# Performance work log

Hardware: AMD Instinct MI355X
Metric: run time of the kernel (lower is better)

Reference implementation:

```python
import jax, jax.numpy as jnp
import numpy as np

EPS_BN = 1e-5
EPS_LN = 1e-5
EPS_L2 = 1e-12


def adder2d(x, w, stride):
    """AdderNet pseudo-conv: out = -sum |x_patch - w| (negative L1 distance).
    x: (N, Cin, H, W); w: (Cout, Cin, kh, kw); no padding, no bias.
    Loops only over the small fixed kernel footprint (<=12 positions) to avoid
    materializing the full im2col L1 tensor at once.
    """
    N, Cin, H, W = x.shape
    Cout, _, kh, kw = w.shape
    sh, sw = stride
    Ho = (H - kh) // sh + 1
    Wo = (W - kw) // sw + 1
    out = jnp.zeros((N, Ho, Wo, Cout), dtype=x.dtype)
    for i in range(kh):
        for j in range(kw):
            # strided slice of the input for this kernel tap: (N, Cin, Ho, Wo)
            xs = x[:, :, i:i + sh * Ho:sh, j:j + sw * Wo:sw]
            xs = jnp.transpose(xs, (0, 2, 3, 1))          # (N, Ho, Wo, Cin)
            wt = w[:, :, i, j]                            # (Cout, Cin)
            # |x - w| summed over Cin -> (N, Ho, Wo, Cout)
            out = out - jnp.abs(xs[:, :, :, None, :] - wt[None, None, None, :, :]).sum(-1)
    return jnp.transpose(out, (0, 3, 1, 2))               # (N, Cout, Ho, Wo)


def bn_relu(x, gamma, beta):
    # training-mode BatchNorm2d (batch statistics, biased var) + ReLU
    mean = x.mean(axis=(0, 2, 3), keepdims=True)
    var = x.var(axis=(0, 2, 3), keepdims=True)
    y = (x - mean) * jax.lax.rsqrt(var + EPS_BN)
    y = y * gamma[None, :, None, None] + beta[None, :, None, None]
    return jax.nn.relu(y)


def setup_inputs() -> dict:
    key = jax.random.key(0)
    ks = jax.random.split(key, 8)
    N = 16
    x = jax.random.normal(ks[0], (N, 1, 196, 3), dtype=jnp.float32)
    w1 = jax.random.normal(ks[1], (128, 1, 6, 1), dtype=jnp.float32) * 0.1
    w2 = jax.random.normal(ks[2], (256, 128, 6, 1), dtype=jnp.float32) * 0.05
    w3 = jax.random.normal(ks[3], (384, 256, 6, 2), dtype=jnp.float32) * 0.05
    g1, b1 = jnp.ones((128,), jnp.float32), jnp.zeros((128,), jnp.float32)
    g2, b2 = jnp.ones((256,), jnp.float32), jnp.zeros((256,), jnp.float32)
    g3, b3 = jnp.ones((384,), jnp.float32), jnp.zeros((384,), jnp.float32)
    Wfc = jax.random.normal(ks[4], (6, 16128), dtype=jnp.float32) * (1.0 / np.sqrt(16128))
    bfc = jax.random.normal(ks[5], (6,), dtype=jnp.float32) * 0.01
    return {"x": x, "w1": w1, "g1": g1, "b1": b1, "w2": w2, "g2": g2, "b2": b2,
            "w3": w3, "g3": g3, "b3": b3, "Wfc": Wfc, "bfc": bfc}


def reference(x, w1, g1, b1, w2, g2, b2, w3, g3, b3, Wfc, bfc):
    h = bn_relu(adder2d(x, w1, (2, 1)), g1, b1)   # (N,128,96,3)
    h = bn_relu(adder2d(h, w2, (2, 1)), g2, b2)   # (N,256,46,3)
    h = bn_relu(adder2d(h, w3, (2, 1)), g3, b3)   # (N,384,21,2)
    h = h.reshape(h.shape[0], -1)                  # (N,16128)
    h = h @ Wfc.T + bfc                            # (N,6)
    # nn.LayerNorm(x.size()) normalizes over ALL dims (batch included), weight=1 bias=0
    mu = h.mean()
    var = h.var()
    h = (h - mu) * jax.lax.rsqrt(var + EPS_LN)
    # F.normalize: per-row L2 normalization
    norm = jnp.sqrt((h * h).sum(axis=1, keepdims=True))
    return h / jnp.maximum(norm, EPS_L2)
```

## Files before the change

kernel.cpp:

```cpp
#include <hip/hip_runtime.h>
#include <math.h>

#define DEVINL __device__ __forceinline__

DEVINL float absadd(float a, float b) {
  float t;
  asm("v_add_f32 %0, |%1|, |%2|" : "=v"(t) : "v"(a), "v"(b));
  return t;
}

template<int NWAVES>
DEVINL void block_reduce_2d(double& a, double& b) {
  #pragma unroll
  for (int off = 32; off > 0; off >>= 1) {
    a += __shfl_down(a, off, 64);
    b += __shfl_down(b, off, 64);
  }
  __shared__ double sa[NWAVES], sb[NWAVES];
  const int tid = threadIdx.x;
  const int wid = tid >> 6;
  if ((tid & 63) == 0) { sa[wid] = a; sb[wid] = b; }
  __syncthreads();
  if (tid == 0) {
    double ta = 0.0, tb = 0.0;
    #pragma unroll
    for (int w = 0; w < NWAVES; ++w) { ta += sa[w]; tb += sb[w]; }
    a = ta; b = tb;
  }
}

__global__ __launch_bounds__(256) void k_conv1(
    const float* __restrict__ x, const float* __restrict__ w1,
    const float* __restrict__ g1, const float* __restrict__ b1,
    float* __restrict__ h1) {
  __shared__ float xlds[9408];
  const int co = blockIdx.x;
  const int tid = threadIdx.x;
  {
    float4* xd = (float4*)xlds;
    const float4* xs = (const float4*)x;
    #pragma unroll
    for (int k = 0; k < 10; ++k) {
      const int f = tid + k * 256;
      if (f < 2352) xd[f] = xs[f];
    }
  }
  float wv[6];
  #pragma unroll
  for (int i = 0; i < 6; ++i) wv[i] = w1[co * 6 + i];
  __syncthreads();

  float vals[18];
  double s = 0.0, sq = 0.0;
  #pragma unroll
  for (int k = 0; k < 18; ++k) {
    const int p = tid + k * 256;
    const int n = p / 288;
    const int r = p - n * 288;
    const int ho = r / 3;
    const int wo = r - ho * 3;
    const float* xb = xlds + n * 588 + (2 * ho) * 3 + wo;
    float e0 = xb[0]  - wv[0];
    float e1 = xb[3]  - wv[1];
    float e2 = xb[6]  - wv[2];
    float e3 = xb[9]  - wv[3];
    float e4 = xb[12] - wv[4];
    float e5 = xb[15] - wv[5];
    const float t0 = absadd(e0, e1);
    const float t1 = absadd(e2, e3);
    const float t2 = absadd(e4, e5);
    const float v = -((t0 + t1) + t2);
    vals[k] = v;
    s += (double)v;
    sq += (double)v * (double)v;
  }
  block_reduce_2d<4>(s, sq);
  __shared__ float ssc, ssh;
  if (tid == 0) {
    const double mean = s * (1.0 / 4608.0);
    const double var  = sq * (1.0 / 4608.0) - mean * mean;
    const float rstd = (float)rsqrt(var + 1e-5);
    const float sc = g1[co] * rstd;
    ssc = sc;
    ssh = b1[co] - (float)mean * sc;
  }
  __syncthreads();
  const float sc = ssc, sh = ssh;
  #pragma unroll
  for (int k = 0; k < 18; ++k) {
    const int p = tid + k * 256;
    const int n = p / 288;
    const int r = p - n * 288;
    const int ho = r / 3;
    const int wo = r - ho * 3;
    h1[((n * 128 + co) * 96 + ho) * 3 + wo] = fmaxf(0.f, fmaf(vals[k], sc, sh));
  }
}

__global__ __launch_bounds__(192) void k_conv2p(
    const float* __restrict__ h1, const float* __restrict__ w2,
    float* __restrict__ part2) {
  __shared__ float wlds[512];
  __shared__ float4 xbuf[2][584];
  const int bx = blockIdx.x;
  const int kc = bx & 7;
  const int rbx = bx >> 3;
  const int cg = rbx & 63;
  const int nh = rbx >> 6;
  const int co0 = cg * 4, ci0 = kc * 16, n0 = nh * 8;
  const int tid = threadIdx.x;
  #pragma unroll
  for (int f = tid; f < 512; f += 192) {
    const int cil = f >> 5, rem = f & 31, c = rem >> 3, kk = rem & 7;
    wlds[f] = (kk < 6) ? w2[(co0 + c) * 768 + (ci0 + cil) * 6 + kk] : 0.f;
  }
  const bool active = tid < 184;
  const int n = tid / 23, hp = tid - n * 23;

  int s_lds[3], s_g[3];
  #pragma unroll
  for (int k = 0; k < 3; ++k) {
    const int f = tid + k * 192;
    const int nn = f / 72, j = f - nn * 72;
    s_lds[k] = nn * 73 + j;
    s_g[k]   = (n0 + nn) * 9216 + j;
  }
  const float4* h1v = (const float4*)h1;

  float acc[4][6];
  #pragma unroll
  for (int c = 0; c < 4; ++c)
    #pragma unroll
    for (int o = 0; o < 6; ++o) acc[c][o] = 0.f;

  float4 r[3];
  #pragma unroll
  for (int k = 0; k < 3; ++k) r[k] = h1v[s_g[k] + ci0 * 72];
  #pragma unroll
  for (int k = 0; k < 3; ++k) xbuf[0][s_lds[k]] = r[k];
  #pragma unroll
  for (int k = 0; k < 3; ++k) r[k] = h1v[s_g[k] + (ci0 + 1) * 72];
  __syncthreads();

  const float4* wl4 = (const float4*)wlds;
  #pragma unroll 1
  for (int ci = 0; ci < 16; ++ci) {
    const float4* cur = xbuf[ci & 1];
    if (ci + 1 < 16) {
      float4* nxt = xbuf[(ci + 1) & 1];
      #pragma unroll
      for (int k = 0; k < 3; ++k) nxt[s_lds[k]] = r[k];
    }
    if (ci + 2 < 16) {
      #pragma unroll
      for (int k = 0; k < 3; ++k) r[k] = h1v[s_g[k] + (ci0 + ci + 2) * 72];
    }
    if (active) {
      const float4* xr = cur + n * 73 + hp * 3;
      float xf[24];
      #pragma unroll
      for (int t = 0; t < 6; ++t) {
        const float4 q = xr[t];
        xf[4 * t + 0] = q.x; xf[4 * t + 1] = q.y; xf[4 * t + 2] = q.z; xf[4 * t + 3] = q.w;
      }
      #pragma unroll
      for (int c = 0; c < 4; ++c) {
        const float4 wa = wl4[(ci * 4 + c) * 2];
        const float4 wb = wl4[(ci * 4 + c) * 2 + 1];
        const float wv[6] = {wa.x, wa.y, wa.z, wa.w, wb.x, wb.y};
        #pragma unroll
        for (int po = 0; po < 2; ++po)
          #pragma unroll
          for (int wo = 0; wo < 3; ++wo) {
            float e0 = xf[(2 * po + 0) * 3 + wo] - wv[0];
            float e1 = xf[(2 * po + 1) * 3 + wo] - wv[1];
            float e2 = xf[(2 * po + 2) * 3 + wo] - wv[2];
            float e3 = xf[(2 * po + 3) * 3 + wo] - wv[3];
            float e4 = xf[(2 * po + 4) * 3 + wo] - wv[4];
            float e5 = xf[(2 * po + 5) * 3 + wo] - wv[5];
            const float t0 = absadd(e0, e1);
            const float t1 = absadd(e2, e3);
            const float t2 = absadd(e4, e5);
            acc[c][po * 3 + wo] += (t0 + t1) + t2;
          }
      }
    }
    __syncthreads();
  }
  if (active) {
    #pragma unroll
    for (int c = 0; c < 4; ++c)
      #pragma unroll
      for (int po = 0; po < 2; ++po)
        #pragma unroll
        for (int wo = 0; wo < 3; ++wo) {
          const int p = (n0 + n) * 138 + (2 * hp + po) * 3 + wo;
          part2[(size_t)(kc * 256 + co0 + c) * 2208 + p] = acc[c][po * 3 + wo];
        }
  }
}

__global__ __launch_bounds__(384) void k_combine2(
    const float* __restrict__ part2, const float* __restrict__ g2,
    const float* __restrict__ b2, float* __restrict__ h2) {
  const int co = blockIdx.x;
  const int tid = threadIdx.x;
  const bool active = tid < 368;
  float v[6];
  double s = 0.0, sq = 0.0;
  #pragma unroll
  for (int k = 0; k < 6; ++k) {
    float sum = 0.f;
    if (active) {
      const int p = tid + k * 368;
      #pragma unroll
      for (int kc = 0; kc < 8; ++kc)
        sum += part2[(size_t)(kc * 256 + co) * 2208 + p];
    }
    const float val = -sum;
    v[k] = val;
    if (active) { s += (double)val; sq += (double)val * (double)val; }
  }
  block_reduce_2d<6>(s, sq);
  __shared__ float ssc, ssh;
  if (tid == 0) {
    const double mean = s * (1.0 / 2208.0);
    const double var  = sq * (1.0 / 2208.0) - mean * mean;
    const float rstd = (float)rsqrt(var + 1e-5);
    const float sc = g2[co] * rstd;
    ssc = sc;
    ssh = b2[co] - (float)mean * sc;
  }
  __syncthreads();
  if (active) {
    const float sc = ssc, sh = ssh;
    #pragma unroll
    for (int k = 0; k < 6; ++k) {
      const int p = tid + k * 368;
      const int n = p / 138, rem = p - n * 138;
      h2[n * 35328 + co * 138 + rem] = fmaxf(0.f, fmaf(v[k], sc, sh));
    }
  }
}

__global__ __launch_bounds__(128) void k_conv3p(
    const float* __restrict__ h2, const float* __restrict__ w3,
    float* __restrict__ part3) {
  __shared__ float wlds[1536];
  __shared__ float2 xbuf[2][560];
  __shared__ float accbuf[64][43];
  const int bx = blockIdx.x;
  const int kc = bx & 15;
  const int rbx = bx >> 4;
  const int cg = rbx % 48;
  const int nh = rbx / 48;
  const int co0 = cg * 8, ci0 = kc * 16, n0 = nh * 8;
  const int tid = threadIdx.x;
  const int wvid = tid >> 6;
  const int lane = tid & 63;
  #pragma unroll
  for (int k = 0; k < 12; ++k) {
    const int f = wvid * 768 + lane + k * 64;
    const int cil = f / 96, rem = f - cil * 96, c = rem / 12, kk = rem - c * 12;
    wlds[f] = w3[(co0 + c) * 3072 + (ci0 + cil) * 12 + kk];
  }
  const int n = lane >> 3, co = lane & 7;

  int s_lds[9], s_g[9];
  const bool v9 = lane < 40;
  #pragma unroll
  for (int k = 0; k < 9; ++k) {
    const int f = lane + k * 64;
    const int nn = f / 69, j = f - nn * 69;
    s_lds[k] = nn * 70 + j;
    s_g[k]   = (n0 + nn) * 17664 + j;
  }
  const float2* h2v = (const float2*)h2;
  const int cibase = ci0 + wvid * 8;

  float acc[42];
  #pragma unroll
  for (int i = 0; i < 42; ++i) acc[i] = 0.f;

  float2 r[9];
  #pragma unroll
  for (int k = 0; k < 8; ++k) r[k] = h2v[s_g[k] + cibase * 69];
  if (v9) r[8] = h2v[s_g[8] + cibase * 69];

  const float2* xrow2 = xbuf[wvid] + n * 70;
  const float4* wl4 = (const float4*)wlds;

  #pragma unroll 1
  for (int cil = 0; cil < 8; ++cil) {
    #pragma unroll
    for (int k = 0; k < 8; ++k) xbuf[wvid][s_lds[k]] = r[k];
    if (v9) xbuf[wvid][s_lds[8]] = r[8];
    if (cil + 1 < 8) {
      #pragma unroll
      for (int k = 0; k < 8; ++k) r[k] = h2v[s_g[k] + (cibase + cil + 1) * 69];
      if (v9) r[8] = h2v[s_g[8] + (cibase + cil + 1) * 69];
    }
    const int cl = wvid * 8 + cil;
    const float4 w0 = wl4[(cl * 8 + co) * 3];
    const float4 w1 = wl4[(cl * 8 + co) * 3 + 1];
    const float4 w2q = wl4[(cl * 8 + co) * 3 + 2];
    const float wv[12] = {w0.x, w0.y, w0.z, w0.w, w1.x, w1.y,
                          w1.z, w1.w, w2q.x, w2q.y, w2q.z, w2q.w};
    float xf[30];
    #pragma unroll
    for (int t = 0; t < 15; ++t) {
      const float2 q = xrow2[t];
      xf[2 * t + 0] = q.x; xf[2 * t + 1] = q.y;
    }
    #pragma unroll
    for (int hot = 0; hot < 7; ++hot) {
      #pragma unroll
      for (int h = 0; h < 3; ++h)
        #pragma unroll
        for (int wo = 0; wo < 2; ++wo) {
          float e0  = xf[(2 * h + 0) * 3 + wo]     - wv[0];
          float e1  = xf[(2 * h + 0) * 3 + wo + 1] - wv[1];
          float e2  = xf[(2 * h + 1) * 3 + wo]     - wv[2];
          float e3  = xf[(2 * h + 1) * 3 + wo + 1] - wv[3];
          float e4  = xf[(2 * h + 2) * 3 + wo]     - wv[4];
          float e5  = xf[(2 * h + 2) * 3 + wo + 1] - wv[5];
          float e6  = xf[(2 * h + 3) * 3 + wo]     - wv[6];
          float e7  = xf[(2 * h + 3) * 3 + wo + 1] - wv[7];
          float e8  = xf[(2 * h + 4) * 3 + wo]     - wv[8];
          float e9  = xf[(2 * h + 4) * 3 + wo + 1] - wv[9];
          float e10 = xf[(2 * h + 5) * 3 + wo]     - wv[10];
          float e11 = xf[(2 * h + 5) * 3 + wo + 1] - wv[11];
          const float t0 = absadd(e0, e1);
          const float t1 = absadd(e2, e3);
          const float t2 = absadd(e4, e5);
          const float t3 = absadd(e6, e7);
          const float t4 = absadd(e8, e9);
          const float t5 = absadd(e10, e11);
          acc[(3 * hot + h) * 2 + wo] += ((t0 + t1) + (t2 + t3)) + (t4 + t5);
        }
      if (hot < 6) {
        #pragma unroll
        for (int t = 0; t < 12; ++t) xf[t] = xf[t + 18];
        #pragma unroll
        for (int t = 0; t < 9; ++t) {
          const float2 q = xrow2[9 * hot + 15 + t];
          xf[12 + 2 * t] = q.x; xf[13 + 2 * t] = q.y;
        }
      }
    }
  }
  if (wvid == 1) {
    #pragma unroll
    for (int i = 0; i < 42; ++i) accbuf[lane][i] = acc[i];
  }
  __syncthreads();
  if (wvid == 0) {
    #pragma unroll
    for (int i = 0; i < 42; ++i) acc[i] += accbuf[lane][i];
    float2* dst = (float2*)(part3 + (size_t)(kc * 384 + co0 + co) * 672 + (n0 + n) * 42);
    #pragma unroll
    for (int k = 0; k < 21; ++k) dst[k] = make_float2(acc[2 * k], acc[2 * k + 1]);
  }
}

__global__ __launch_bounds__(384) void k_combine3(
    const float* __restrict__ part3, const float* __restrict__ g3,
    const float* __restrict__ b3, float* __restrict__ h3) {
  const int co = blockIdx.x;
  const int tid = threadIdx.x;
  const bool active = tid < 336;
  float v[2];
  double s = 0.0, sq = 0.0;
  #pragma unroll
  for (int k = 0; k < 2; ++k) {
    float sum = 0.f;
    if (active) {
      const int p = tid + k * 336;
      #pragma unroll
      for (int kc = 0; kc < 16; ++kc)
        sum += part3[(size_t)(kc * 384 + co) * 672 + p];
    }
    const float val = -sum;
    v[k] = val;
    if (active) { s += (double)val; sq += (double)val * (double)val; }
  }
  block_reduce_2d<6>(s, sq);
  __shared__ float ssc, ssh;
  if (tid == 0) {
    const double mean = s * (1.0 / 672.0);
    const double var  = sq * (1.0 / 672.0) - mean * mean;
    const float rstd = (float)rsqrt(var + 1e-5);
    const float sc = g3[co] * rstd;
    ssc = sc;
    ssh = b3[co] - (float)mean * sc;
  }
  __syncthreads();
  if (active) {
    const float sc = ssc, sh = ssh;
    #pragma unroll
    for (int k = 0; k < 2; ++k) {
      const int p = tid + k * 336;
      const int n = p / 42, rem = p - n * 42;
      h3[n * 16128 + co * 42 + rem] = fmaxf(0.f, fmaf(v[k], sc, sh));
    }
  }
}

__global__ __launch_bounds__(256) void k_fcp(
    const float* __restrict__ h3, const float* __restrict__ Wfc,
    float* __restrict__ hfcp) {
  const int bx = blockIdx.x;
  const int pair = bx >> 2, q = bx & 3;
  const int n = pair / 6, o = pair - n * 6;
  const float4* xr = (const float4*)(h3 + n * 16128) + q * 1008;
  const float4* wr = (const float4*)(Wfc + o * 16128) + q * 1008;
  float sacc = 0.f;
  for (int k = threadIdx.x; k < 1008; k += 256) {
    const float4 xv = xr[k];
    const float4 wv = wr[k];
    sacc += xv.x * wv.x + xv.y * wv.y + xv.z * wv.z + xv.w * wv.w;
  }
  double d = (double)sacc, dummy = 0.0;
  block_reduce_2d<4>(d, dummy);
  if (threadIdx.x == 0) hfcp[bx] = (float)d;
}

__global__ __launch_bounds__(128) void k_final(
    const float* __restrict__ hfcp, const float* __restrict__ bfc,
    float* __restrict__ out) {
  __shared__ float ys[96];
  __shared__ float params[2];
  const int tid = threadIdx.x;
  float v = 0.f;
  if (tid < 96) {
    v = hfcp[tid * 4 + 0] + hfcp[tid * 4 + 1] + hfcp[tid * 4 + 2] + hfcp[tid * 4 + 3]
        + bfc[tid % 6];
    ys[tid] = v;
  }
  __syncthreads();
  if (tid == 0) {
    double s = 0.0, sq = 0.0;
    for (int i = 0; i < 96; ++i) { const double t = (double)ys[i]; s += t; sq += t * t; }
    const double mu = s / 96.0;
    const double var = sq / 96.0 - mu * mu;
    params[0] = (float)mu;
    params[1] = (float)rsqrt(var + 1e-5);
  }
  __syncthreads();
  const float y = (v - params[0]) * params[1];
  __syncthreads();
  if (tid < 96) ys[tid] = y;
  __syncthreads();
  if (tid < 96) {
    const int n = tid / 6;
    float ss = 0.f;
    #pragma unroll
    for (int k = 0; k < 6; ++k) { const float t = ys[n * 6 + k]; ss += t * t; }
    const float norm = sqrtf(ss);
    out[tid] = y / fmaxf(norm, 1e-12f);
  }
}

extern "C" void kernel_launch(void* const* d_in, const int* in_sizes, int n_in,
                              void* d_out, int out_size, void* d_ws, size_t ws_size,
                              hipStream_t stream) {
  const float* x   = (const float*)d_in[0];
  const float* w1  = (const float*)d_in[1];
  const float* g1  = (const float*)d_in[2];
  const float* b1  = (const float*)d_in[3];
  const float* w2  = (const float*)d_in[4];
  const float* g2  = (const float*)d_in[5];
  const float* b2  = (const float*)d_in[6];
  const float* w3  = (const float*)d_in[7];
  const float* g3  = (const float*)d_in[8];
  const float* b3  = (const float*)d_in[9];
  const float* Wfc = (const float*)d_in[10];
  const float* bfc = (const float*)d_in[11];

  float* ws   = (float*)d_ws;
  float* h1   = ws;
  float* h2   = h1 + 589824;
  float* h3   = h2 + 565248;
  float* hfcp = h3 + 258048;
  float* part = hfcp + 384;
  float* out  = (float*)d_out;

  k_conv1   <<<128, 256, 0, stream>>>(x, w1, g1, b1, h1);
  k_conv2p  <<<1024, 192, 0, stream>>>(h1, w2, part);
  k_combine2<<<256, 384, 0, stream>>>(part, g2, b2, h2);
  k_conv3p  <<<1536, 128, 0, stream>>>(h2, w3, part);
  k_combine3<<<384, 384, 0, stream>>>(part, g3, b3, h3);
  k_fcp     <<<384, 256, 0, stream>>>(h3, Wfc, hfcp);
  k_final   <<<1, 128, 0, stream>>>(hfcp, bfc, out);
}
```

Before: 120.1 us.

## Restructure conv2 adder kernel so each thread owns a full output column with a sliding window

The layer-2 adder conv kernel is reorganised. Each thread now handles one (batch, output channel) pair across 23 output rows and 3 columns, and reuses input rows through a register sliding window. Each block covers 8 output channels and half of the output height. Each of the two waves works on its own half of the input-channel chunk with per-wave LDS buffers and no per-iteration block barriers, and the two partial sums are combined through shared memory at the end. This removes redundant LDS input loads and block-wide syncs, but costs a large register footprint (69 accumulators), more LDS per block, fewer threads per block, and uncoalesced per-thread stores of contiguous rows.

```diff
diff --git a/kernel.cpp b/kernel.cpp
--- a/kernel.cpp
+++ b/kernel.cpp
@@ -97,106 +97,112 @@
   }
 }
 
-__global__ __launch_bounds__(192) void k_conv2p(
+__global__ __launch_bounds__(128) void k_conv2p(
     const float* __restrict__ h1, const float* __restrict__ w2,
     float* __restrict__ part2) {
-  __shared__ float wlds[512];
-  __shared__ float4 xbuf[2][584];
+  __shared__ float wlds[1024];
+  __shared__ float2 xbuf[2][616];
+  __shared__ float accbuf[64][71];
   const int bx = blockIdx.x;
   const int kc = bx & 7;
   const int rbx = bx >> 3;
-  const int cg = rbx & 63;
-  const int nh = rbx >> 6;
-  const int co0 = cg * 4, ci0 = kc * 16, n0 = nh * 8;
-  const int tid = threadIdx.x;
-  #pragma unroll
-  for (int f = tid; f < 512; f += 192) {
-    const int cil = f >> 5, rem = f & 31, c = rem >> 3, kk = rem & 7;
+  const int cg = rbx & 31;
+  const int rbx2 = rbx >> 5;
+  const int hoh = rbx2 & 1;
+  const int nh = rbx2 >> 1;
+  const int co0 = cg * 8, ci0 = kc * 16, n0 = nh * 8;
+  const int tid = threadIdx.x;
+  const int wvid = tid >> 6;
+  const int lane = tid & 63;
+  #pragma unroll
+  for (int k = 0; k < 8; ++k) {
+    const int f = wvid * 512 + lane + k * 64;
+    const int cil = f >> 6, rem = f & 63, c = rem >> 3, kk = rem & 7;
     wlds[f] = (kk < 6) ? w2[(co0 + c) * 768 + (ci0 + cil) * 6 + kk] : 0.f;
   }
-  const bool active = tid < 184;
-  const int n = tid / 23, hp = tid - n * 23;
-
-  int s_lds[3], s_g[3];
-  #pragma unroll
-  for (int k = 0; k < 3; ++k) {
-    const int f = tid + k * 192;
-    const int nn = f / 72, j = f - nn * 72;
-    s_lds[k] = nn * 73 + j;
-    s_g[k]   = (n0 + nn) * 9216 + j;
-  }
-  const float4* h1v = (const float4*)h1;
-
-  float acc[4][6];
-  #pragma unroll
-  for (int c = 0; c < 4; ++c)
-    #pragma unroll
-    for (int o = 0; o < 6; ++o) acc[c][o] = 0.f;
-
-  float4 r[3];
-  #pragma unroll
-  for (int k = 0; k < 3; ++k) r[k] = h1v[s_g[k] + ci0 * 72];
-  #pragma unroll
-  for (int k = 0; k < 3; ++k) xbuf[0][s_lds[k]] = r[k];
-  #pragma unroll
-  for (int k = 0; k < 3; ++k) r[k] = h1v[s_g[k] + (ci0 + 1) * 72];
-  __syncthreads();
-
+  const int n = lane >> 3, co = lane & 7;
+
+  int s_lds[10], s_g[10];
+  const bool v10 = lane < 24;
+  #pragma unroll
+  for (int k = 0; k < 10; ++k) {
+    const int f = lane + k * 64;
+    const int nn = f / 75, j = f - nn * 75;
+    s_lds[k] = nn * 77 + j;
+    s_g[k]   = (n0 + nn) * 18432 + 69 * hoh + j;
+  }
+  const float2* h1v = (const float2*)h1;
+  const int cibase = ci0 + wvid * 8;
+
+  float acc[69];
+  #pragma unroll
+  for (int i = 0; i < 69; ++i) acc[i] = 0.f;
+
+  float2 r[10];
+  #pragma unroll
+  for (int k = 0; k < 9; ++k) r[k] = h1v[s_g[k] + cibase * 144];
+  if (v10) r[9] = h1v[s_g[9] + cibase * 144];
+
+  const float2* xrow2 = xbuf[wvid] + n * 77;
   const float4* wl4 = (const float4*)wlds;
+
   #pragma unroll 1
-  for (int ci = 0; ci < 16; ++ci) {
-    const float4* cur = xbuf[ci & 1];
-    if (ci + 1 < 16) {
-      float4* nxt = xbuf[(ci + 1) & 1];
+  for (int cil = 0; cil < 8; ++cil) {
+    #pragma unroll
+    for (int k = 0; k < 9; ++k) xbuf[wvid][s_lds[k]] = r[k];
+    if (v10) xbuf[wvid][s_lds[9]] = r[9];
+    if (cil + 1 < 8) {
       #pragma unroll
-      for (int k = 0; k < 3; ++k) nxt[s_lds[k]] = r[k];
-    }
-    if (ci + 2 < 16) {
-      #pragma unroll
-      for (int k = 0; k < 3; ++k) r[k] = h1v[s_g[k] + (ci0 + ci + 2) * 72];
-    }
-    if (active) {
-      const float4* xr = cur + n * 73 + hp * 3;
-      float xf[24];
-      #pragma unroll
-      for (int t = 0; t < 6; ++t) {
-        const float4 q = xr[t];
-        xf[4 * t + 0] = q.x; xf[4 * t + 1] = q.y; xf[4 * t + 2] = q.z; xf[4 * t + 3] = q.w;
+      for (int k = 0; k < 9; ++k) r[k] = h1v[s_g[k] + (cibase + cil + 1) * 144];
+      if (v10) r[9] = h1v[s_g[9] + (cibase + cil + 1) * 144];
+    }
+    const int cl = wvid * 8 + cil;
+    const float4 wa = wl4[(cl * 8 + co) * 2];
+    const float4 wb = wl4[(cl * 8 + co) * 2 + 1];
+    const float wv[6] = {wa.x, wa.y, wa.z, wa.w, wb.x, wb.y};
+    float xf[18];
+    #pragma unroll
+    for (int t = 0; t < 9; ++t) {
+      const float2 q = xrow2[t];
+      xf[2 * t] = q.x; xf[2 * t + 1] = q.y;
+    }
+    #pragma unroll
+    for (int h = 0; h < 23; ++h) {
+      if (h > 0) {
+        #pragma unroll
+        for (int t = 0; t < 12; ++t) xf[t] = xf[t + 6];
+        #pragma unroll
+        for (int t = 0; t < 3; ++t) {
+          const float2 q = xrow2[3 * h + 6 + t];
+          xf[12 + 2 * t] = q.x; xf[13 + 2 * t] = q.y;
+        }
       }
       #pragma unroll
-      for (int c = 0; c < 4; ++c) {
-        const float4 wa = wl4[(ci * 4 + c) * 2];
-        const float4 wb = wl4[(ci * 4 + c) * 2 + 1];
-        const float wv[6] = {wa.x, wa.y, wa.z, wa.w, wb.x, wb.y};
-        #pragma unroll
-        for (int po = 0; po < 2; ++po)
-          #pragma unroll
-          for (int wo = 0; wo < 3; ++wo) {
-            float e0 = xf[(2 * po + 0) * 3 + wo] - wv[0];
-            float e1 = xf[(2 * po + 1) * 3 + wo] - wv[1];
-            float e2 = xf[(2 * po + 2) * 3 + wo] - wv[2];
-            float e3 = xf[(2 * po + 3) * 3 + wo] - wv[3];
-            float e4 = xf[(2 * po + 4) * 3 + wo] - wv[4];
-            float e5 = xf[(2 * po + 5) * 3 + wo] - wv[5];
-            const float t0 = absadd(e0, e1);
-            const float t1 = absadd(e2, e3);
-            const float t2 = absadd(e4, e5);
-            acc[c][po * 3 + wo] += (t0 + t1) + t2;
-          }
+      for (int wo = 0; wo < 3; ++wo) {
+        float e0 = xf[0  + wo] - wv[0];
+        float e1 = xf[3  + wo] - wv[1];
+        float e2 = xf[6  + wo] - wv[2];
+        float e3 = xf[9  + wo] - wv[3];
+        float e4 = xf[12 + wo] - wv[4];
+        float e5 = xf[15 + wo] - wv[5];
+        const float t0 = absadd(e0, e1);
+        const float t1 = absadd(e2, e3);
+        const float t2 = absadd(e4, e5);
+        acc[h * 3 + wo] += (t0 + t1) + t2;
       }
     }
-    __syncthreads();
-  }
-  if (active) {
-    #pragma unroll
-    for (int c = 0; c < 4; ++c)
-      #pragma unroll
-      for (int po = 0; po < 2; ++po)
-        #pragma unroll
-        for (int wo = 0; wo < 3; ++wo) {
-          const int p = (n0 + n) * 138 + (2 * hp + po) * 3 + wo;
-          part2[(size_t)(kc * 256 + co0 + c) * 2208 + p] = acc[c][po * 3 + wo];
-        }
+  }
+  if (wvid == 1) {
+    #pragma unroll
+    for (int i = 0; i < 69; ++i) accbuf[lane][i] = acc[i];
+  }
+  __syncthreads();
+  if (wvid == 0) {
+    #pragma unroll
+    for (int i = 0; i < 69; ++i) acc[i] += accbuf[lane][i];
+    float* dst = part2 + (size_t)(kc * 256 + co0 + co) * 2208 + (n0 + n) * 138 + 69 * hoh;
+    #pragma unroll
+    for (int i = 0; i < 69; ++i) dst[i] = acc[i];
   }
 }
 
@@ -486,7 +492,7 @@
   float* out  = (float*)d_out;
 
   k_conv1   <<<128, 256, 0, stream>>>(x, w1, g1, b1, h1);
-  k_conv2p  <<<1024, 192, 0, stream>>>(h1, w2, part);
+  k_conv2p  <<<1024, 128, 0, stream>>>(h1, w2, part);
   k_combine2<<<256, 384, 0, stream>>>(part, g2, b2, h2);
   k_conv3p  <<<1536, 128, 0, stream>>>(h2, w3, part);
   k_combine3<<<384, 384, 0, stream>>>(part, g3, b3, h3);
```

Measured after the change: 108.9 us. 1.1x faster.
